# Optimization experiments

Hardware: AMD Instinct MI355X
Metric: run time of the kernel (lower is better)

The kernel has to match this reference:

```python
import jax, jax.numpy as jnp
import numpy as np

EPS = 1e-3  # keras LayerNormalization default epsilon
D = 128     # sub_band_feature_dim
# band structure for input_freq_dim=257, sr=16000 (freq_resolution=31.25 Hz)
GROUPS = [(8, 4, 0), (12, 8, 32), (8, 16, 128)]  # (n_bands, bins_per_band, start_bin)


def setup_inputs() -> dict:
    key = jax.random.key(0)
    ks = jax.random.split(key, 8)
    B, T = 16, 1000
    inp = {"inputs": jax.random.normal(ks[0], (B, T, 257), dtype=jnp.float32)}
    for gi, (n, c, _) in enumerate(GROUPS, start=1):
        kW = jax.random.fold_in(ks[1], gi)
        inp[f"gamma{gi}"] = jnp.ones((n, c), dtype=jnp.float32)
        inp[f"beta{gi}"] = jnp.zeros((n, c), dtype=jnp.float32)
        inp[f"W{gi}"] = jax.random.normal(kW, (n, c, D), dtype=jnp.float32) * (1.0 / np.sqrt(c))
        inp[f"b{gi}"] = jnp.zeros((n, D), dtype=jnp.float32)
    return inp


def _group(x, start, n, c, gamma, beta, W, b):
    # x: [B,T,F] -> slice and view as [B,T,n_bands,c]
    B, T, _ = x.shape
    xs = x[:, :, start:start + n * c].reshape(B, T, n, c)
    mean = jnp.mean(xs, axis=-1, keepdims=True)
    var = jnp.mean(jnp.square(xs - mean), axis=-1, keepdims=True)
    xn = (xs - mean) / jnp.sqrt(var + EPS) * gamma + beta  # per-band gamma/beta [n,c]
    # per-band dense: [B,T,n,c] x [n,c,D] -> [B,T,n,D]
    return jnp.einsum('btgc,gcd->btgd', xn, W) + b[None, None]


def reference(inputs, gamma1, beta1, W1, b1, gamma2, beta2, W2, b2, gamma3, beta3, W3, b3):
    outs = []
    params = [(gamma1, beta1, W1, b1), (gamma2, beta2, W2, b2), (gamma3, beta3, W3, b3)]
    for (n, c, start), (g, bt, W, b) in zip(GROUPS, params):
        outs.append(_group(inputs, start, n, c, g, bt, W, b))
    return jnp.concatenate(outs, axis=2)  # [B,T,28,128]
```

## Files before the change

### kernel.cpp

```cpp
#include <hip/hip_runtime.h>

#define EPS 1e-3f

template<int C>
__global__ __launch_bounds__(256)
void bandsplit_group(const float* __restrict__ x, int BT,
                     const float* __restrict__ W_all,
                     const float* __restrict__ gamma,
                     const float* __restrict__ beta,
                     const float* __restrict__ bias,
                     int start0, int band0, int nb,
                     float* __restrict__ out)
{
    __shared__ float xn_lds[64 * C];
    const int l     = blockIdx.x % nb;
    const int bt0   = (blockIdx.x / nb) * 64;
    const int band  = band0 + l;
    const int start = start0 + l * C;
    const int tid   = threadIdx.x;

    const int d4 = (tid & 31) * 4;
    float4 w[C];
#pragma unroll
    for (int jj = 0; jj < C; ++jj)
        w[jj] = *(const float4*)(W_all + (l * C + jj) * 128 + d4);
    const float4 bias4 = *(const float4*)(bias + l * 128 + d4);

    const int j  = tid & (C - 1);
    const int rl = tid / C;
    const int RPP = 256 / C;
    const float gam = gamma[l * C + j];
    const float bet = beta[l * C + j];
    const float inv_c = 1.0f / (float)C;
#pragma unroll
    for (int p = 0; p < 64 / RPP + ((64 % RPP) ? 1 : 0); ++p) {
        const int row = p * RPP + rl;
        const float xv = x[(size_t)(bt0 + row) * 257 + start + j];
        float s = xv, sq = xv * xv;
#pragma unroll
        for (int m = 1; m < C; m <<= 1) {
            s  += __shfl_xor(s,  m);
            sq += __shfl_xor(sq, m);
        }
        const float mean = s * inv_c;
        const float var  = sq * inv_c - mean * mean;
        xn_lds[row * C + j] = (xv - mean) * rsqrtf(var + EPS) * gam + bet;
    }
    __syncthreads();

    const int rr = tid >> 5;
#pragma unroll
    for (int i = 0; i < 8; ++i) {
        const int row = i * 8 + rr;
        float4 acc = bias4;
#pragma unroll
        for (int jj = 0; jj < C; ++jj) {
            const float xv = xn_lds[row * C + jj];
            acc.x += xv * w[jj].x;
            acc.y += xv * w[jj].y;
            acc.z += xv * w[jj].z;
            acc.w += xv * w[jj].w;
        }
        *(float4*)(out + ((size_t)(bt0 + row) * 28 + band) * 128 + d4) = acc;
    }
}

extern "C" void kernel_launch(void* const* d_in, const int* in_sizes, int n_in,
                              void* d_out, int out_size, void* d_ws, size_t ws_size,
                              hipStream_t stream) {
    const float* x   = (const float*)d_in[0];
    const float* g1  = (const float*)d_in[1];
    const float* be1 = (const float*)d_in[2];
    const float* W1  = (const float*)d_in[3];
    const float* b1  = (const float*)d_in[4];
    const float* g2  = (const float*)d_in[5];
    const float* be2 = (const float*)d_in[6];
    const float* W2  = (const float*)d_in[7];
    const float* b2  = (const float*)d_in[8];
    const float* g3  = (const float*)d_in[9];
    const float* be3 = (const float*)d_in[10];
    const float* W3  = (const float*)d_in[11];
    const float* b3  = (const float*)d_in[12];
    float* out = (float*)d_out;

    const int BT    = in_sizes[0] / 257;
    const int tiles = (BT + 63) / 64;

    bandsplit_group<4><<<dim3(tiles * 8),  dim3(256), 0, stream>>>(
        x, BT, W1, g1, be1, b1, 0,   0,  8,  out);
    bandsplit_group<8><<<dim3(tiles * 12), dim3(256), 0, stream>>>(
        x, BT, W2, g2, be2, b2, 32,  8,  12, out);
    bandsplit_group<16><<<dim3(tiles * 8), dim3(256), 0, stream>>>(
        x, BT, W3, g3, be3, b3, 128, 20, 8 == 8 ? 8 : 8, out);
}
```

Baseline: 266.7 us.

## Fold LayerNorm affine into weights and stream rows without shared memory

A small prep kernel folds gamma into W and beta·W plus bias into a per-band bias vector, stored in workspace. The main kernels drop the LDS staging and the barrier. Each warp now reads a row's C inputs directly (broadcast loads), computes mean and variance in registers and accumulates the dense output for R rows. Blocks get smaller row tiles, giving more blocks. This adds a kernel launch and redundant per-lane input loads in exchange for removing the shared-memory round trip and the sync.

```diff
diff --git a/kernel.cpp b/kernel.cpp
--- a/kernel.cpp
+++ b/kernel.cpp
@@ -2,66 +2,79 @@
 
 #define EPS 1e-3f
 
-template<int C>
+__global__ __launch_bounds__(128)
+void prep_kernel(const float* __restrict__ g1, const float* __restrict__ be1,
+                 const float* __restrict__ W1, const float* __restrict__ b1,
+                 const float* __restrict__ g2, const float* __restrict__ be2,
+                 const float* __restrict__ W2, const float* __restrict__ b2,
+                 const float* __restrict__ g3, const float* __restrict__ be3,
+                 const float* __restrict__ W3, const float* __restrict__ b3,
+                 float* __restrict__ wp, float* __restrict__ bp)
+{
+    const int band = blockIdx.x;
+    const int d    = threadIdx.x;
+    int C, l; const float *W, *ga, *be, *bi; float* wdst;
+    if (band < 8)       { C = 4;  l = band;      W = W1; ga = g1; be = be1; bi = b1; wdst = wp + l * 4 * 128; }
+    else if (band < 20) { C = 8;  l = band - 8;  W = W2; ga = g2; be = be2; bi = b2; wdst = wp + 4096 + l * 8 * 128; }
+    else                { C = 16; l = band - 20; W = W3; ga = g3; be = be3; bi = b3; wdst = wp + 16384 + l * 16 * 128; }
+    float acc = bi[l * 128 + d];
+    for (int jj = 0; jj < C; ++jj) {
+        const float Wv = W[(l * C + jj) * 128 + d];
+        wdst[jj * 128 + d] = Wv * ga[l * C + jj];
+        acc += be[l * C + jj] * Wv;
+    }
+    bp[band * 128 + d] = acc;
+}
+
+template<int C, int R>
 __global__ __launch_bounds__(256)
-void bandsplit_group(const float* __restrict__ x, int BT,
-                     const float* __restrict__ W_all,
-                     const float* __restrict__ gamma,
-                     const float* __restrict__ beta,
-                     const float* __restrict__ bias,
-                     int start0, int band0, int nb,
-                     float* __restrict__ out)
+void bandsplit_stream(const float* __restrict__ x, int BT,
+                      const float* __restrict__ wpg,
+                      const float* __restrict__ bp,
+                      int start0, int band0, int nb,
+                      float* __restrict__ out)
 {
-    __shared__ float xn_lds[64 * C];
     const int l     = blockIdx.x % nb;
-    const int bt0   = (blockIdx.x / nb) * 64;
+    const int rt    = blockIdx.x / nb;
     const int band  = band0 + l;
     const int start = start0 + l * C;
     const int tid   = threadIdx.x;
+    const int d4    = (tid & 31) * 4;
+    const int rg    = tid >> 5;
+    const int r0    = rt * (8 * R) + rg * R;
 
-    const int d4 = (tid & 31) * 4;
     float4 w[C];
 #pragma unroll
     for (int jj = 0; jj < C; ++jj)
-        w[jj] = *(const float4*)(W_all + (l * C + jj) * 128 + d4);
-    const float4 bias4 = *(const float4*)(bias + l * 128 + d4);
+        w[jj] = *(const float4*)(wpg + (l * C + jj) * 128 + d4);
+    const float4 b4 = *(const float4*)(bp + band * 128 + d4);
+    const float inv_c = 1.0f / (float)C;
 
-    const int j  = tid & (C - 1);
-    const int rl = tid / C;
-    const int RPP = 256 / C;
-    const float gam = gamma[l * C + j];
-    const float bet = beta[l * C + j];
-    const float inv_c = 1.0f / (float)C;
 #pragma unroll
-    for (int p = 0; p < 64 / RPP + ((64 % RPP) ? 1 : 0); ++p) {
-        const int row = p * RPP + rl;
-        const float xv = x[(size_t)(bt0 + row) * 257 + start + j];
-        float s = xv, sq = xv * xv;
+    for (int k = 0; k < R; ++k) {
+        const int bt = r0 + k;
+        if (bt < BT) {
+            const float* xr = x + (size_t)bt * 257 + start;
+            float xv[C];
 #pragma unroll
-        for (int m = 1; m < C; m <<= 1) {
-            s  += __shfl_xor(s,  m);
-            sq += __shfl_xor(sq, m);
+            for (int jj = 0; jj < C; ++jj) xv[jj] = xr[jj];
+            float s = 0.f, sq = 0.f;
+#pragma unroll
+            for (int jj = 0; jj < C; ++jj) { s += xv[jj]; sq += xv[jj] * xv[jj]; }
+            const float mean = s * inv_c;
+            const float var  = sq * inv_c - mean * mean;
+            const float rstd = rsqrtf(var + EPS);
+            float4 acc = b4;
+#pragma unroll
+            for (int jj = 0; jj < C; ++jj) {
+                const float z = (xv[jj] - mean) * rstd;
+                acc.x += z * w[jj].x;
+                acc.y += z * w[jj].y;
+                acc.z += z * w[jj].z;
+                acc.w += z * w[jj].w;
+            }
+            *(float4*)(out + ((size_t)bt * 28 + band) * 128 + d4) = acc;
         }
-        const float mean = s * inv_c;
-        const float var  = sq * inv_c - mean * mean;
-        xn_lds[row * C + j] = (xv - mean) * rsqrtf(var + EPS) * gam + bet;
-    }
-    __syncthreads();
-
-    const int rr = tid >> 5;
-#pragma unroll
-    for (int i = 0; i < 8; ++i) {
-        const int row = i * 8 + rr;
-        float4 acc = bias4;
-#pragma unroll
-        for (int jj = 0; jj < C; ++jj) {
-            const float xv = xn_lds[row * C + jj];
-            acc.x += xv * w[jj].x;
-            acc.y += xv * w[jj].y;
-            acc.z += xv * w[jj].z;
-            acc.w += xv * w[jj].w;
-        }
-        *(float4*)(out + ((size_t)(bt0 + row) * 28 + band) * 128 + d4) = acc;
     }
 }
 
@@ -83,13 +96,20 @@
     const float* b3  = (const float*)d_in[12];
     float* out = (float*)d_out;
 
-    const int BT    = in_sizes[0] / 257;
-    const int tiles = (BT + 63) / 64;
+    float* wp = (float*)d_ws;
+    float* bp = wp + 32768;
 
-    bandsplit_group<4><<<dim3(tiles * 8),  dim3(256), 0, stream>>>(
-        x, BT, W1, g1, be1, b1, 0,   0,  8,  out);
-    bandsplit_group<8><<<dim3(tiles * 12), dim3(256), 0, stream>>>(
-        x, BT, W2, g2, be2, b2, 32,  8,  12, out);
-    bandsplit_group<16><<<dim3(tiles * 8), dim3(256), 0, stream>>>(
-        x, BT, W3, g3, be3, b3, 128, 20, 8 == 8 ? 8 : 8, out);
+    prep_kernel<<<dim3(28), dim3(128), 0, stream>>>(
+        g1, be1, W1, b1, g2, be2, W2, b2, g3, be3, W3, b3, wp, bp);
+
+    const int BT = in_sizes[0] / 257;
+
+    const int t32 = (BT + 31) / 32;
+    const int t16 = (BT + 15) / 16;
+    bandsplit_stream<4, 4><<<dim3(8  * t32), dim3(256), 0, stream>>>(
+        x, BT, wp,         bp, 0,   0,  8,  out);
+    bandsplit_stream<8, 4><<<dim3(12 * t32), dim3(256), 0, stream>>>(
+        x, BT, wp + 4096,  bp, 32,  8,  12, out);
+    bandsplit_stream<16, 2><<<dim3(8 * t16), dim3(256), 0, stream>>>(
+        x, BT, wp + 16384, bp, 128, 20, 8,  out);
 }
```

Measured after the change: 313.2 us. 17.4% more time.
